# Kernel tuning notes

Hardware: AMD Instinct MI355X
Metric: run time of the kernel (lower is better)

The kernel has to match this reference:

```python
import jax, jax.numpy as jnp
import numpy as np

NUM_HEADS = 12
HEAD_SIZE = 64  # hidden_size // num_heads


def setup_inputs() -> dict:
    key = jax.random.key(0)
    ks = jax.random.split(key, 4)
    B, S, H = 2, 2048, 768
    return {
        "hidden_states": jax.random.normal(ks[0], (B, S, H), dtype=jnp.float32),
        "attention_mask": jnp.ones((B, S), dtype=jnp.int32),
        "Wq": jax.random.normal(ks[1], (H, H), dtype=jnp.float32) * 0.02,
        "bq": jnp.zeros((H,), dtype=jnp.float32),
        "Wk": jax.random.normal(ks[2], (H, H), dtype=jnp.float32) * 0.02,
        "bk": jnp.zeros((H,), dtype=jnp.float32),
        "Wv": jax.random.normal(ks[3], (H, H), dtype=jnp.float32) * 0.02,
        "bv": jnp.zeros((H,), dtype=jnp.float32),
    }


def reference(hidden_states, attention_mask, Wq, bq, Wk, bk, Wv, bv):
    B, S, H = hidden_states.shape
    nh, hs = NUM_HEADS, HEAD_SIZE

    def to_heads(x):  # [B,S,H] -> [nh,B,S,hs] (matches to_multi_head)
        return x.reshape(B, S, nh, hs).transpose(2, 0, 1, 3)

    # torch Linear: y = x @ W.T + b
    q = to_heads(hidden_states @ Wq.T + bq)
    k = to_heads(hidden_states @ Wk.T + bk)
    v = to_heads(hidden_states @ Wv.T + bv)

    scores = jnp.einsum("hbqd,hbkd->hbqk", q, k) / jnp.float32(hs) ** 0.5
    # mask: 1 -> attend, 0 -> -inf; broadcast over query dim
    m = 1.0 - attention_mask.astype(scores.dtype)
    add = jnp.where(m != 0.0, -jnp.inf, 0.0)[None, :, None, :]  # [1,B,1,S]
    probs = jax.nn.softmax(scores + add, axis=-1)
    # dropout is identity in eval mode
    out = jnp.einsum("hbqk,hbkd->hbqd", probs, v)
    # from_multi_head: [nh,B,S,hs] -> [B,S,H]
    return out.transpose(1, 2, 0, 3).reshape(B, S, H)
```

## Files before the change

### kernel.cpp

```cpp
#include <hip/hip_runtime.h>
#include <hip/hip_bf16.h>

#define BATCH 2
#define SEQ   2048
#define HID   768
#define NH    12
#define HS    64
#define MROWS (BATCH*SEQ)
#define N3    (3*HID)
#define HB    (NH*BATCH)

typedef __attribute__((ext_vector_type(8))) short short8;
typedef __attribute__((ext_vector_type(4))) float floatx4;

#define QSCALE 0.1803368801111204f

__device__ __forceinline__ unsigned short f2bf(float x){
  __hip_bfloat16 h = __float2bfloat16(x);
  return __builtin_bit_cast(unsigned short, h);
}
__device__ __forceinline__ unsigned int f2bf2(float lo, float hi){
  return (unsigned int)f2bf(lo) | ((unsigned int)f2bf(hi) << 16);
}
__device__ __forceinline__ unsigned int f2bf2_rhu(float lo, float hi){
  unsigned int a = __builtin_bit_cast(unsigned int, lo) + 0x8000u;
  unsigned int b = __builtin_bit_cast(unsigned int, hi) + 0x8000u;
  return __builtin_amdgcn_perm(b, a, 0x07060302u);
}
__device__ __forceinline__ float fast_exp2(float x){
  return __builtin_amdgcn_exp2f(x);
}
__device__ __forceinline__ void glds16(const unsigned short* g, unsigned short* l){
  __builtin_amdgcn_global_load_lds(
    (const __attribute__((address_space(1))) unsigned int*)g,
    (__attribute__((address_space(3))) unsigned int*)l, 16, 0, 0);
}

__global__ void f2bf_all_kernel(const float* __restrict__ X,
                                const float* __restrict__ Wq,
                                const float* __restrict__ Wk,
                                const float* __restrict__ Wv,
                                const int* __restrict__ mask,
                                unsigned short* __restrict__ Xb,
                                unsigned short* __restrict__ Wb,
                                float* __restrict__ maskaddG,
                                unsigned int* __restrict__ flagsG){
  const int XQ = MROWS*HID/4;
  const int WQ = HID*HID/4;
  const int NB = (XQ + 3*WQ)/256;
  const int tid = threadIdx.x;
  if(blockIdx.x == NB){
    for(int i=tid;i<BATCH*SEQ;i+=256) maskaddG[i] = mask[i] ? 0.f : -1e30f;
    if(tid < 2) flagsG[tid] = 0u;
    __syncthreads();
    if(tid < BATCH*32){
      int b = tid >> 5, t = tid & 31;
      const int* mrow = mask + b*SEQ + t*64;
      int any = 0;
      for(int i=0;i<64;i++) any |= (mrow[i]==0);
      if(any) atomicOr(&flagsG[b], 1u << t);
    }
    return;
  }
  int i = blockIdx.x * 256 + tid;
  const float* src; unsigned short* dst; int off;
  if(i < XQ){ src = X; dst = Xb; off = i; }
  else {
    int j = i - XQ;
    int w = j / WQ; off = j - w*WQ;
    src = (w==0) ? Wq : (w==1) ? Wk : Wv;
    dst = Wb + (size_t)w*HID*HID;
  }
  float4 v = reinterpret_cast<const float4*>(src)[off];
  ushort4 o;
  o.x = f2bf(v.x); o.y = f2bf(v.y); o.z = f2bf(v.z); o.w = f2bf(v.w);
  reinterpret_cast<ushort4*>(dst)[off] = o;
}

__global__ __launch_bounds__(256) void qkv_gemm_kernel(
    const unsigned short* __restrict__ Xb,
    const unsigned short* __restrict__ Wb,
    const float* __restrict__ bq, const float* __restrict__ bk, const float* __restrict__ bv,
    unsigned short* __restrict__ Qb, unsigned short* __restrict__ Kb,
    unsigned short* __restrict__ Vtb)
{
  __shared__ __align__(16) union {
    struct { unsigned short A[2][128][32]; unsigned short B[2][128][32]; } s;
    unsigned short T[4][64][72];
  } u;
  const int m0 = blockIdx.y << 7;
  const int n0 = blockIdx.x << 7;
  const int tid  = threadIdx.x;
  const int wave = tid >> 6, lane = tid & 63;
  const int wr = wave >> 1, wc = wave & 1;
  const int quad = lane >> 4, l15 = lane & 15;

  const unsigned short* gsrc[4];
  unsigned short* ldst[4];
  #pragma unroll
  for(int p=0;p<4;p++){
    int ck  = ((p&1)<<8) + tid;
    int row = ck>>2, c = ck&3, pc = c ^ (row&3);
    if(p<2){ gsrc[p] = Xb + (size_t)(m0+row)*HID + (pc<<3); ldst[p] = &u.s.A[0][row][c<<3]; }
    else   { gsrc[p] = Wb + (size_t)(n0+row)*HID + (pc<<3); ldst[p] = &u.s.B[0][row][c<<3]; }
  }

  floatx4 acc[4][4];
  #pragma unroll
  for(int i=0;i<4;i++)
    #pragma unroll
    for(int j=0;j<4;j++) acc[i][j] = (floatx4){0.f,0.f,0.f,0.f};

  auto stage = [&](int buf, int k0){
    const int bo = buf*(128*32);
    #pragma unroll
    for(int p=0;p<4;p++) glds16(gsrc[p] + k0, ldst[p] + bo);
  };

  stage(0, 0);
  __syncthreads();

  const int swa = l15 & 3;
  for(int t=0;t<HID/32;t++){
    const int buf = t & 1;
    if(t < HID/32 - 1) stage(buf^1, (t+1)*32);
    short8 a[4], b[4];
    #pragma unroll
    for(int i=0;i<4;i++)
      a[i] = *reinterpret_cast<const short8*>(&u.s.A[buf][wr*64+i*16+l15][(quad^swa)<<3]);
    #pragma unroll
    for(int j=0;j<4;j++)
      b[j] = *reinterpret_cast<const short8*>(&u.s.B[buf][wc*64+j*16+l15][(quad^swa)<<3]);
    #pragma unroll
    for(int i=0;i<4;i++)
      #pragma unroll
      for(int j=0;j<4;j++)
        acc[i][j] = __builtin_amdgcn_mfma_f32_16x16x32_bf16(a[i], b[j], acc[i][j], 0, 0, 0);
    __syncthreads();
  }

  const int which = n0 / HID;
  const int nbase = n0 - which*HID + wc*64;
  const int head  = nbase >> 6;
  const int b_    = m0 >> 11;
  const int hb    = head*BATCH + b_;
  const int s0    = (m0 & 2047) + wr*64;
  if(which < 2){
    unsigned short* dst = which==0 ? Qb : Kb;
    const float* bias = which==0 ? bq : bk;
    const float scale = which==0 ? QSCALE : 1.0f;
    #pragma unroll
    for(int j=0;j<4;j++){
      const float bb = bias[nbase + j*16 + l15];
      #pragma unroll
      for(int i=0;i<4;i++)
        #pragma unroll
        for(int r=0;r<4;r++)
          u.T[wave][i*16 + quad*4 + r][j*16 + l15] = f2bf((acc[i][j][r] + bb)*scale);
    }
    #pragma unroll
    for(int p=0;p<8;p++){
      const int row = p*8 + (lane>>3), dc = (lane&7)*8;
      uint4 v = *reinterpret_cast<const uint4*>(&u.T[wave][row][dc]);
      *reinterpret_cast<uint4*>(dst + ((size_t)(hb<<11) + s0 + row)*HS + dc) = v;
    }
  } else {
    #pragma unroll
    for(int j=0;j<4;j++){
      const float bb = bv[nbase + j*16 + l15];
      #pragma unroll
      for(int i=0;i<4;i++){
        uint2 pk;
        pk.x = f2bf2(acc[i][j][0]+bb, acc[i][j][1]+bb);
        pk.y = f2bf2(acc[i][j][2]+bb, acc[i][j][3]+bb);
        *reinterpret_cast<uint2*>(&u.T[wave][j*16+l15][i*16 + quad*4]) = pk;
      }
    }
    #pragma unroll
    for(int p=0;p<8;p++){
      const int d = p*8 + (lane>>3), cm = lane & 7;
      uint4 v = *reinterpret_cast<const uint4*>(&u.T[wave][d][cm*8]);
      *reinterpret_cast<uint4*>(Vtb + ((size_t)(hb*HS) + d)*SEQ + s0 + cm*8) = v;
    }
  }
}

__global__ __launch_bounds__(256) void attn_kernel(
    const unsigned short* __restrict__ Qb,
    const unsigned short* __restrict__ Kb,
    const unsigned short* __restrict__ Vtb,
    const float* __restrict__ maskaddG,
    const unsigned int* __restrict__ flagsG,
    float* __restrict__ out)
{
  __shared__ __align__(16) unsigned short Ks2 [2][64][64];
  __shared__ __align__(16) unsigned short Vts2[2][64][64];
  __shared__ __align__(16) unsigned short Ps2 [4][16][68];

  const int bid = blockIdx.x;
  const int hb = bid >> 5, qt = bid & 31, q0 = qt << 6;
  const int tid = threadIdx.x, wave = tid >> 6, lane = tid & 63;
  const int quad = lane >> 4, l15 = lane & 15;
  const int b_ = hb & 1, head = hb >> 1;

  const unsigned short* gK[2]; const unsigned short* gV[2];
  unsigned short* lK[2]; unsigned short* lV[2];
  #pragma unroll
  for(int p=0;p<2;p++){
    int ck = (p<<8) + tid;
    int row = ck>>3, c = ck&7, pc = c ^ (row&7);
    gK[p] = Kb  + ((size_t)(hb<<11) + row)*HS + (pc<<3);
    lK[p] = &Ks2[0][row][c<<3];
    gV[p] = Vtb + ((size_t)(hb*HS) + row)*SEQ + (pc<<3);
    lV[p] = &Vts2[0][row][c<<3];
  }
  auto stage = [&](int buf, int k0){
    const int bo = buf*(64*64);
    #pragma unroll
    for(int p=0;p<2;p++){
      glds16(gK[p] + (size_t)k0*HS, lK[p] + bo);
      glds16(gV[p] + k0,           lV[p] + bo);
    }
  };

  stage(0, 0);

  short8 a_q[2];
  {
    const unsigned short* qsrc = Qb + ((size_t)(hb<<11) + q0 + wave*16 + l15)*HS;
    a_q[0] = *reinterpret_cast<const short8*>(qsrc + quad*8);
    a_q[1] = *reinterpret_cast<const short8*>(qsrc + 32 + quad*8);
  }
  const unsigned int fl = flagsG[b_];

  float lsum4[4] = {0.f,0.f,0.f,0.f};
  floatx4 o_acc[4];
  #pragma unroll
  for(int dt=0;dt<4;dt++) o_acc[dt] = (floatx4){0.f,0.f,0.f,0.f};

  __syncthreads();

  const int sw = l15 & 7;
  for(int t=0;t<SEQ/64;t++){
    const int buf = t & 1, k0 = t << 6;
    if(t < SEQ/64 - 1) stage(buf^1, k0 + 64);

    const unsigned short (*Kst)[64] = Ks2[buf];
    const unsigned short (*Vst)[64] = Vts2[buf];

    floatx4 st[4];
    #pragma unroll
    for(int kt=0;kt<4;kt++){
      st[kt] = (floatx4){0.f,0.f,0.f,0.f};
      #pragma unroll
      for(int c=0;c<2;c++){
        short8 kf = *reinterpret_cast<const short8*>(
            &Kst[kt*16 + l15][(((c<<2)+quad)^sw)<<3]);
        st[kt] = __builtin_amdgcn_mfma_f32_16x16x32_bf16(kf, a_q[c], st[kt], 0, 0, 0);
      }
    }

    const bool masked = (fl >> t) & 1u;
    #pragma unroll
    for(int kt=0;kt<4;kt++){
      float p0,p1,p2,p3;
      if(!masked){
        p0 = fast_exp2(st[kt][0]); p1 = fast_exp2(st[kt][1]);
        p2 = fast_exp2(st[kt][2]); p3 = fast_exp2(st[kt][3]);
      } else {
        float4 ma = *reinterpret_cast<const float4*>(
            maskaddG + (b_<<11) + k0 + kt*16 + quad*4);
        p0 = fast_exp2(st[kt][0] + ma.x); p1 = fast_exp2(st[kt][1] + ma.y);
        p2 = fast_exp2(st[kt][2] + ma.z); p3 = fast_exp2(st[kt][3] + ma.w);
      }
      lsum4[0] += p0; lsum4[1] += p1; lsum4[2] += p2; lsum4[3] += p3;
      uint2 pk;
      pk.x = f2bf2_rhu(p0, p1);
      pk.y = f2bf2_rhu(p2, p3);
      *reinterpret_cast<uint2*>(&Ps2[wave][l15][kt*16 + quad*4]) = pk;
    }

    short8 ap0, ap1;
    {
      unsigned long long x0 = *reinterpret_cast<const unsigned long long*>(&Ps2[wave][l15][quad*8]);
      unsigned long long x1 = *reinterpret_cast<const unsigned long long*>(&Ps2[wave][l15][quad*8 + 4]);
      unsigned long long y0 = *reinterpret_cast<const unsigned long long*>(&Ps2[wave][l15][32 + quad*8]);
      unsigned long long y1 = *reinterpret_cast<const unsigned long long*>(&Ps2[wave][l15][32 + quad*8 + 4]);
      union { unsigned long long u[2]; short8 s; } cv0, cv1;
      cv0.u[0] = x0; cv0.u[1] = x1;
      cv1.u[0] = y0; cv1.u[1] = y1;
      ap0 = cv0.s; ap1 = cv1.s;
    }
    #pragma unroll
    for(int dt=0;dt<4;dt++){
      short8 bv0 = *reinterpret_cast<const short8*>(&Vst[dt*16 + l15][(quad^sw)<<3]);
      short8 bv1 = *reinterpret_cast<const short8*>(&Vst[dt*16 + l15][((4+quad)^sw)<<3]);
      o_acc[dt] = __builtin_amdgcn_mfma_f32_16x16x32_bf16(ap0, bv0, o_acc[dt], 0, 0, 0);
      o_acc[dt] = __builtin_amdgcn_mfma_f32_16x16x32_bf16(ap1, bv1, o_acc[dt], 0, 0, 0);
    }
    __syncthreads();
  }

  float lsum = (lsum4[0]+lsum4[1]) + (lsum4[2]+lsum4[3]);
  lsum += __shfl_xor(lsum, 16);
  lsum += __shfl_xor(lsum, 32);
  float linv[4];
  #pragma unroll
  for(int r=0;r<4;r++) linv[r] = 1.0f / __shfl(lsum, quad*4 + r);

  #pragma unroll
  for(int dt=0;dt<4;dt++){
    #pragma unroll
    for(int r=0;r<4;r++){
      const int srow = q0 + wave*16 + quad*4 + r;
      out[((size_t)(b_<<11) + srow)*HID + (head<<6) + dt*16 + l15] =
        o_acc[dt][r] * linv[r];
    }
  }
}

extern "C" void kernel_launch(void* const* d_in, const int* in_sizes, int n_in,
                              void* d_out, int out_size, void* d_ws, size_t ws_size,
                              hipStream_t stream) {
  const float* X    = (const float*)d_in[0];
  const int*   mask = (const int*)  d_in[1];
  const float* Wq   = (const float*)d_in[2];
  const float* bq   = (const float*)d_in[3];
  const float* Wk   = (const float*)d_in[4];
  const float* bk   = (const float*)d_in[5];
  const float* Wv   = (const float*)d_in[6];
  const float* bv   = (const float*)d_in[7];
  float* out = (float*)d_out;

  char* ws = (char*)d_ws;
  unsigned short* Xb  = (unsigned short*)ws;
  unsigned short* Wb  = Xb  + (size_t)MROWS*HID;
  unsigned short* Qb  = Wb  + (size_t)N3*HID;
  unsigned short* Kb  = Qb  + (size_t)HB*SEQ*HS;
  unsigned short* Vtb = Kb  + (size_t)HB*SEQ*HS;
  float* maskaddG = (float*)(Vtb + (size_t)HB*SEQ*HS);
  unsigned int* flagsG = (unsigned int*)(maskaddG + MROWS);

  const int total_quads = (MROWS*HID + 3*HID*HID)/4;
  f2bf_all_kernel<<<total_quads/256 + 1, 256, 0, stream>>>(
      X, Wq, Wk, Wv, mask, Xb, Wb, maskaddG, flagsG);

  qkv_gemm_kernel<<<dim3(N3/128, MROWS/128), 256, 0, stream>>>(
      Xb, Wb, bq, bk, bv, Qb, Kb, Vtb);

  attn_kernel<<<HB*32, 256, 0, stream>>>(
      Qb, Kb, Vtb, maskaddG, flagsG, out);
}
```

Baseline: 163.2 us.

## Split attention keys across waves with transposed QK and cross-wave output reduction

```diff
diff --git a/kernel.cpp b/kernel.cpp
--- a/kernel.cpp
+++ b/kernel.cpp
@@ -11,7 +11,17 @@
 #define HB    (NH*BATCH)
 
 typedef __attribute__((ext_vector_type(8))) short short8;
+typedef __attribute__((ext_vector_type(4))) short short4v;
 typedef __attribute__((ext_vector_type(4))) float floatx4;
+
+#ifndef __has_builtin
+#define __has_builtin(x) 0
+#endif
+#if __has_builtin(__builtin_amdgcn_mfma_f32_16x16x16bf16_1k)
+#define HAVE_K16 1
+#else
+#define HAVE_K16 0
+#endif
 
 #define QSCALE 0.1803368801111204f
 
@@ -185,6 +195,160 @@
   }
 }
 
+#if HAVE_K16
+__global__ __launch_bounds__(256, 3) void attn_kernel(
+    const unsigned short* __restrict__ Qb,
+    const unsigned short* __restrict__ Kb,
+    const unsigned short* __restrict__ Vtb,
+    const float* __restrict__ maskaddG,
+    const unsigned int* __restrict__ flagsG,
+    float* __restrict__ out)
+{
+  __shared__ __align__(16) union {
+    struct { unsigned short K[2][64][64]; unsigned short V[2][64][64]; } s;
+    float Os[64][68];
+  } sm;
+  __shared__ float lsumS[4][64];
+
+  const int bid = blockIdx.x;
+  const int hb = bid >> 5, qt = bid & 31, q0 = qt << 6;
+  const int tid = threadIdx.x, wave = tid >> 6, lane = tid & 63;
+  const int quad = lane >> 4, l15 = lane & 15;
+  const int b_ = hb & 1, head = hb >> 1;
+
+  const unsigned short* gK[2]; const unsigned short* gV[2];
+  unsigned short* lK[2]; unsigned short* lV[2];
+  #pragma unroll
+  for(int p=0;p<2;p++){
+    int ck = (p<<8) + tid;
+    int row = ck>>3, c = ck&7, pc = c ^ (row&7);
+    gK[p] = Kb  + ((size_t)(hb<<11) + row)*HS + (pc<<3);
+    lK[p] = &sm.s.K[0][row][c<<3];
+    gV[p] = Vtb + ((size_t)(hb*HS) + row)*SEQ + (pc<<3);
+    lV[p] = &sm.s.V[0][row][c<<3];
+  }
+  auto stage = [&](int buf, int k0){
+    const int bo = buf*(64*64);
+    #pragma unroll
+    for(int p=0;p<2;p++){
+      glds16(gK[p] + (size_t)k0*HS, lK[p] + bo);
+      glds16(gV[p] + k0,           lV[p] + bo);
+    }
+  };
+
+  stage(0, 0);
+
+  short8 a_q[4][2];
+  #pragma unroll
+  for(int f=0;f<4;f++){
+    const unsigned short* qsrc = Qb + ((size_t)(hb<<11) + q0 + f*16 + l15)*HS;
+    a_q[f][0] = *reinterpret_cast<const short8*>(qsrc + quad*8);
+    a_q[f][1] = *reinterpret_cast<const short8*>(qsrc + 32 + quad*8);
+  }
+  const unsigned int fl = flagsG[b_];
+
+  float lsum4[4] = {0.f,0.f,0.f,0.f};
+  floatx4 o_acc[4][4];
+  #pragma unroll
+  for(int f=0;f<4;f++)
+    #pragma unroll
+    for(int g=0;g<4;g++) o_acc[f][g] = (floatx4){0.f,0.f,0.f,0.f};
+
+  __syncthreads();
+
+  const int sw = l15 & 7;
+  const int krow = wave*16 + l15;
+  const int vch = ((wave<<1) + (quad>>1)) ^ sw;
+  const int voff = (vch<<3) + ((quad&1)<<2);
+
+  for(int t=0;t<SEQ/64;t++){
+    const int buf = t & 1, k0 = t << 6;
+    if(t < SEQ/64 - 1) stage(buf^1, k0 + 64);
+
+    const unsigned short (*Kst)[64] = sm.s.K[buf];
+    const unsigned short (*Vst)[64] = sm.s.V[buf];
+
+    short8 kf0 = *reinterpret_cast<const short8*>(&Kst[krow][(quad^sw)<<3]);
+    short8 kf1 = *reinterpret_cast<const short8*>(&Kst[krow][((4+quad)^sw)<<3]);
+
+    floatx4 st[4];
+    #pragma unroll
+    for(int f=0;f<4;f++) st[f] = (floatx4){0.f,0.f,0.f,0.f};
+    #pragma unroll
+    for(int f=0;f<4;f++) st[f] = __builtin_amdgcn_mfma_f32_16x16x32_bf16(kf0, a_q[f][0], st[f], 0, 0, 0);
+    #pragma unroll
+    for(int f=0;f<4;f++) st[f] = __builtin_amdgcn_mfma_f32_16x16x32_bf16(kf1, a_q[f][1], st[f], 0, 0, 0);
+
+    float4 ma = (float4){0.f,0.f,0.f,0.f};
+    if((fl >> t) & 1u)
+      ma = *reinterpret_cast<const float4*>(maskaddG + (b_<<11) + k0 + wave*16 + quad*4);
+
+    short4v pA[4];
+    #pragma unroll
+    for(int f=0;f<4;f++){
+      float p0 = fast_exp2(st[f][0] + ma.x);
+      float p1 = fast_exp2(st[f][1] + ma.y);
+      float p2 = fast_exp2(st[f][2] + ma.z);
+      float p3 = fast_exp2(st[f][3] + ma.w);
+      lsum4[f] += (p0+p1) + (p2+p3);
+      union { unsigned int u[2]; short4v s; } pk;
+      pk.u[0] = f2bf2_rhu(p0, p1);
+      pk.u[1] = f2bf2_rhu(p2, p3);
+      pA[f] = pk.s;
+    }
+
+    #pragma unroll
+    for(int g=0;g<4;g++){
+      short4v bvg = *reinterpret_cast<const short4v*>(&Vst[g*16 + l15][voff]);
+      #pragma unroll
+      for(int f=0;f<4;f++)
+        o_acc[f][g] = __builtin_amdgcn_mfma_f32_16x16x16bf16_1k(pA[f], bvg, o_acc[f][g], 0, 0, 0);
+    }
+    __syncthreads();
+  }
+
+  #pragma unroll
+  for(int f=0;f<4;f++){
+    lsum4[f] += __shfl_xor(lsum4[f], 16);
+    lsum4[f] += __shfl_xor(lsum4[f], 32);
+  }
+  if(lane < 16){
+    #pragma unroll
+    for(int f=0;f<4;f++) lsumS[wave][f*16 + lane] = lsum4[f];
+  }
+
+  #pragma unroll
+  for(int w=0;w<4;w++){
+    if(wave == w){
+      #pragma unroll
+      for(int f=0;f<4;f++)
+        #pragma unroll
+        for(int g=0;g<4;g++){
+          floatx4* dst = reinterpret_cast<floatx4*>(&sm.Os[g*16 + l15][f*16 + quad*4]);
+          if(w == 0) *dst = o_acc[f][g];
+          else      *dst = *dst + o_acc[f][g];
+        }
+    }
+    __syncthreads();
+  }
+
+  {
+    const int q = tid >> 2, dch = (tid & 3) << 4;
+    const float linv = 1.0f /
+      (lsumS[0][q] + lsumS[1][q] + lsumS[2][q] + lsumS[3][q]);
+    float* orow = out + ((size_t)(b_<<11) + q0 + q)*HID + (head<<6) + dch;
+    #pragma unroll
+    for(int c4=0;c4<4;c4++){
+      float4 o;
+      o.x = sm.Os[dch + c4*4 + 0][q] * linv;
+      o.y = sm.Os[dch + c4*4 + 1][q] * linv;
+      o.z = sm.Os[dch + c4*4 + 2][q] * linv;
+      o.w = sm.Os[dch + c4*4 + 3][q] * linv;
+      reinterpret_cast<float4*>(orow)[c4] = o;
+    }
+  }
+}
+#else
 __global__ __launch_bounds__(256) void attn_kernel(
     const unsigned short* __restrict__ Qb,
     const unsigned short* __restrict__ Kb,
@@ -224,7 +388,6 @@
   };
 
   stage(0, 0);
-
   short8 a_q[2];
   {
     const unsigned short* qsrc = Qb + ((size_t)(hb<<11) + q0 + wave*16 + l15)*HS;
@@ -318,6 +481,7 @@
     }
   }
 }
+#endif
 
 extern "C" void kernel_launch(void* const* d_in, const int* in_sizes, int n_in,
                               void* d_out, int out_size, void* d_ws, size_t ws_size,
```

Result: no change. 160.8 us (-1.5%).
